# Kernel tuning notes

Hardware: AMD Instinct MI355X
Metric: run time of the kernel (lower is better)

Reference implementation:

```python
import jax, jax.numpy as jnp
import numpy as np

B, C, H, W = 2, 48, 64, 64
EPS = 1e-5
ROW = [0, 0, 0, H // 4, H // 4, H // 4, H // 2, H // 2, H // 2]
COL = [0, W // 4, W // 2] * 3


def setup_inputs() -> dict:
    key = jax.random.key(0)
    ks = iter(jax.random.split(key, 40))
    s = 1.0 / np.sqrt(C)  # keep unscaled-softmax logits sane
    def rn(shape, scale=1.0):
        return jax.random.normal(next(ks), shape, jnp.float32) * scale
    def ru(shape):
        return jax.random.uniform(next(ks), shape, jnp.float32, 0.5, 1.5)
    return dict(
        input_feature=rn((B, C, H, W)), feat_b=rn((B, C, H, W)),
        feat_c=rn((B, C, H, W)), feat_d=rn((B, C, H, W)),
        W_fa_all=rn((C, C), s), W_fb_all=rn((C, C), s),
        W_fc_all=rn((C, C), s), W_fd_all=rn((C, C), s),
        W_fa=rn((9, C, C), s), W_fb=rn((9, C, C), s),
        W_fc=rn((9, C, C), s), W_fd=rn((9, C, C), s),
        fuse_w=rn((C, 4 * C), s), fuse_b=rn((C,), 0.1),
        fuse_g=ru((C,)), fuse_bb=rn((C,), 0.1), fuse_m=rn((C,), 0.1), fuse_v=ru((C,)),
        fuseP_w=rn((9, C, 4 * C), s), fuseP_b=rn((9, C), 0.1),
        fuseP_g=ru((9, C)), fuseP_bb=rn((9, C), 0.1), fuseP_m=rn((9, C), 0.1), fuseP_v=ru((9, C)),
        gamma_all=rn(()), gamma_p=rn((9,)),
        out_w=rn((C, C, 3, 3), s / 3.0), out_b=rn((C,), 0.1),
        out_g=ru((C,)), out_bb=rn((C,), 0.1), out_m=rn((C,), 0.1), out_v=ru((C,)),
    )


def _attn(q, k, v):
    # q,k,v: [..., C, N] -> energy [..., N, N]; non-standard softmax(max - energy)
    e = jnp.einsum('...cn,...cm->...nm', q, k)
    e = jnp.max(e, axis=-1, keepdims=True) - e
    a = jax.nn.softmax(e, axis=-1)
    return jnp.einsum('...cn,...nm->...cm', v, a)  # torch.matmul(v, attention)


def reference(input_feature, feat_b, feat_c, feat_d,
              W_fa_all, W_fb_all, W_fc_all, W_fd_all,
              W_fa, W_fb, W_fc, W_fd,
              fuse_w, fuse_b, fuse_g, fuse_bb, fuse_m, fuse_v,
              fuseP_w, fuseP_b, fuseP_g, fuseP_bb, fuseP_m, fuseP_v,
              gamma_all, gamma_p,
              out_w, out_b, out_g, out_bb, out_m, out_v):
    h2, w2 = H // 2, W // 2
    N = H * W
    # ---- global branch: channel-wise Linear (bias=False) applied over spatial tokens
    fa = jnp.einsum('dc,bcn->bdn', W_fa_all, input_feature.reshape(B, C, N))
    fb = jnp.einsum('dc,bcn->bdn', W_fb_all, feat_b.reshape(B, C, N))
    fc = jnp.einsum('dc,bcn->bdn', W_fc_all, feat_c.reshape(B, C, N))
    fd = jnp.einsum('dc,bcn->bdn', W_fd_all, feat_d.reshape(B, C, N))
    cat = jnp.concatenate([_attn(fa, fa, fa), _attn(fa, fb, fb),
                           _attn(fa, fc, fc), _attn(fa, fd, fd)], axis=1)
    cat = cat.reshape(B, 4 * C, H, W)
    y = jnp.einsum('oc,bchw->bohw', fuse_w, cat) + fuse_b[None, :, None, None]
    y = (y - fuse_m[:, None, None]) * (fuse_g / jnp.sqrt(fuse_v + EPS))[:, None, None] + fuse_bb[:, None, None]
    atten_all = jax.nn.relu(y)  # Dropout2d is identity at eval
    # ---- 9 overlapping patch branches, vectorized over the patch axis p
    def crops(x):
        return jnp.stack([x[:, :, r:r + h2, c:c + w2] for r, c in zip(ROW, COL)], 0).reshape(9, B, C, h2 * w2)
    pa = jnp.einsum('pdc,pbcn->pbdn', W_fa, crops(input_feature))
    pb = jnp.einsum('pdc,pbcn->pbdn', W_fb, crops(feat_b))
    pc = jnp.einsum('pdc,pbcn->pbdn', W_fc, crops(feat_c))
    pd = jnp.einsum('pdc,pbcn->pbdn', W_fd, crops(feat_d))
    pcat = jnp.concatenate([_attn(pa, pa, pa), _attn(pa, pb, pb),
                            _attn(pa, pc, pc), _attn(pa, pd, pd)], axis=2)
    pcat = pcat.reshape(9, B, 4 * C, h2, w2)
    py = jnp.einsum('poc,pbchw->pbohw', fuseP_w, pcat) + fuseP_b[:, None, :, None, None]
    py = ((py - fuseP_m[:, None, :, None, None])
          * (fuseP_g / jnp.sqrt(fuseP_v + EPS))[:, None, :, None, None]
          + fuseP_bb[:, None, :, None, None])
    patch_out = 0.5 * gamma_p[:, None, None, None, None] * jax.nn.relu(py)
    # ---- combine (overlapping patch regions accumulate additively, as in torch +=)
    out = input_feature + gamma_all * atten_all
    for i, (r, c) in enumerate(zip(ROW, COL)):
        out = out.at[:, :, r:r + h2, c:c + w2].add(patch_out[i])
    # ---- to_out: 3x3 conv + BN(eval) + ReLU
    z = jax.lax.conv_general_dilated(out, out_w, (1, 1), 'SAME',
                                     dimension_numbers=('NCHW', 'OIHW', 'NCHW'))
    z = z + out_b[None, :, None, None]
    z = (z - out_m[:, None, None]) * (out_g / jnp.sqrt(out_v + EPS))[:, None, None] + out_bb[:, None, None]
    return jax.nn.relu(z)
```

## Files before the change

### kernel.cpp

```cpp
#include <hip/hip_runtime.h>
#include <math.h>

typedef _Float16 f16;
typedef f16 f16x8 __attribute__((ext_vector_type(8)));
typedef float f32x4 __attribute__((ext_vector_type(4)));

namespace {
constexpr int B_ = 2, C_ = 48, H_ = 64, W_ = 64;
constexpr int N_ = H_ * W_;
constexpr int NP_ = 1024;
constexpr int C4_ = 4 * C_;
constexpr float EPS_ = 1e-5f;
constexpr float L2E_ = 1.44269504f;
constexpr float REFL2_ = -25.0f * 1.44269504f;
}

#define MFMA32(a, b, c) __builtin_amdgcn_mfma_f32_16x16x32_f16((a), (b), (c), 0, 0, 0)

__device__ inline float fast_exp2(float x) {
#if __has_builtin(__builtin_amdgcn_exp2f)
  return __builtin_amdgcn_exp2f(x);
#else
  float r;
  asm("v_exp_f32 %0, %1" : "=v"(r) : "v"(x));
  return r;
#endif
}

__device__ __attribute__((always_inline)) void proj_body(
    const float* __restrict__ xb, const float* __restrict__ Ws,
    f16* __restrict__ pnb, size_t pn_stride, f16* __restrict__ ptb) {
  float acc[48];
#pragma unroll
  for (int d = 0; d < 48; ++d) acc[d] = 0.f;
  for (int c0 = 0; c0 < 48; c0 += 4) {
    float xv0 = xb[(size_t)(c0 + 0) * 4096];
    float xv1 = xb[(size_t)(c0 + 1) * 4096];
    float xv2 = xb[(size_t)(c0 + 2) * 4096];
    float xv3 = xb[(size_t)(c0 + 3) * 4096];
#pragma unroll
    for (int d = 0; d < 48; ++d) {
      const float4 wv = *(const float4*)&Ws[d * 48 + c0];
      acc[d] = fmaf(wv.x, xv0, fmaf(wv.y, xv1, fmaf(wv.z, xv2, fmaf(wv.w, xv3, acc[d]))));
    }
  }
#pragma unroll
  for (int d = 0; d < 48; ++d) pnb[(size_t)d * pn_stride] = (f16)acc[d];
#pragma unroll
  for (int s = 0; s < 6; ++s) {
    f16x8 v;
#pragma unroll
    for (int j = 0; j < 8; ++j) v[j] = (f16)acc[s * 8 + j];
    *(f16x8*)(ptb + s * 8) = v;
  }
  f16x8 zv = {0, 0, 0, 0, 0, 0, 0, 0};
  *(f16x8*)(ptb + 48) = zv;
  *(f16x8*)(ptb + 56) = zv;
}

__global__ __launch_bounds__(256) void k_proj_all(
    const float* __restrict__ x0, const float* __restrict__ x1,
    const float* __restrict__ x2, const float* __restrict__ x3,
    const float* __restrict__ w0, const float* __restrict__ w1,
    const float* __restrict__ w2, const float* __restrict__ w3,
    const float* __restrict__ wp0, const float* __restrict__ wp1,
    const float* __restrict__ wp2, const float* __restrict__ wp3,
    f16* __restrict__ pgn, f16* __restrict__ pgt,
    f16* __restrict__ ppn, f16* __restrict__ ppt) {
  __shared__ float Ws[48 * 48];
  int tid = threadIdx.x;
  int bid = blockIdx.x;
  if (bid < 128) {
    int bx = bid & 15, b = (bid >> 4) & 1, X = bid >> 5;
    const float* xp = X == 0 ? x0 : X == 1 ? x1 : X == 2 ? x2 : x3;
    const float* wp = X == 0 ? w0 : X == 1 ? w1 : X == 2 ? w2 : w3;
    for (int i = tid; i < 2304; i += 256) Ws[i] = wp[i];
    __syncthreads();
    int n = bx * 256 + tid;
    int z2 = X * 2 + b;
    proj_body(xp + (size_t)b * 48 * 4096 + n, Ws,
              pgn + ((size_t)z2 * 48) * 4096 + n, 4096,
              pgt + ((size_t)z2 * 4096 + n) * 64);
  } else {
    int pid = bid - 128;
    int bx = pid & 3;
    int rest = pid >> 2;
    int p = rest % 9;
    int zb = rest / 9;
    int X = zb >> 1, b = zb & 1;
    const float* xp = X == 0 ? x0 : X == 1 ? x1 : X == 2 ? x2 : x3;
    const float* wp = (X == 0 ? wp0 : X == 1 ? wp1 : X == 2 ? wp2 : wp3) + (size_t)p * 2304;
    for (int i = tid; i < 2304; i += 256) Ws[i] = wp[i];
    __syncthreads();
    int t = bx * 256 + tid;
    int r0 = (p / 3) * 16, c0w = (p % 3) * 16;
    int rr = r0 + (t >> 5), cc = c0w + (t & 31);
    int z9 = (X * 2 + b) * 9 + p;
    proj_body(xp + (size_t)b * 48 * 4096 + rr * 64 + cc, Ws,
              ppn + ((size_t)z9 * 48) * 1024 + t, 1024,
              ppt + ((size_t)z9 * 1024 + t) * 64);
  }
}

template <int NT, int NSPLIT, bool PATCH>
__device__ __attribute__((always_inline)) void stats_body(
    const f16* __restrict__ qT_all, const f16* __restrict__ kT_all,
    float* __restrict__ stp, int bx, int by, uint4* Ks) {
  constexpr int MTI = (NT / NSPLIT) / 64;
  int tid = threadIdx.x, wave = tid >> 6, lane = tid & 63, g = lane >> 4, lm = lane & 15;
  int ms = by % NSPLIT, z = by / NSPLIT;
  const f16* qT;
  if (PATCH) {
    int b = (z / 9) % 2, p = z % 9;
    qT = qT_all + ((size_t)(b * 9 + p)) * NT * 64;
  } else {
    int b = z & 1;
    qT = qT_all + (size_t)b * NT * 64;
  }
  const f16* kT = kT_all + (size_t)z * NT * 64;
  int n0 = bx * 128 + wave * 16;
  f16x8 aq0a = *(const f16x8*)(qT + (size_t)(n0 + lm) * 64 + g * 8);
  f16x8 aq1a = *(const f16x8*)(qT + (size_t)(n0 + lm) * 64 + 32 + g * 8);
  f16x8 aq0b = *(const f16x8*)(qT + (size_t)(n0 + 64 + lm) * 64 + g * 8);
  f16x8 aq1b = *(const f16x8*)(qT + (size_t)(n0 + 64 + lm) * 64 + 32 + g * 8);
  const int s0r = tid >> 3, s0c = (tid & 7) * 8;
  const int sw0 = tid ^ ((tid >> 3) & 7);
  const int sw1 = (tid + 256) ^ (((tid + 256) >> 3) & 7);
  const int swl = lm & 7;
  const int c0i = g ^ swl, c1i = (4 + g) ^ swl;
  int t_beg = ms * MTI;
  {
    const f16* src = kT + (size_t)t_beg * 64 * 64;
    Ks[sw0] = *(const uint4*)(src + (size_t)s0r * 64 + s0c);
    Ks[sw1] = *(const uint4*)(src + (size_t)(s0r + 32) * 64 + s0c);
  }
  __syncthreads();
  float zsa[4] = {0.f, 0.f, 0.f, 0.f};
  float zsb[4] = {0.f, 0.f, 0.f, 0.f};
  for (int mt = 0; mt < MTI; ++mt) {
    int cur = mt & 1;
    bool pf = (mt + 1 < MTI);
    uint4 k0v, k1v;
    if (pf) {
      const f16* src = kT + (size_t)(t_beg + mt + 1) * 64 * 64;
      k0v = *(const uint4*)(src + (size_t)s0r * 64 + s0c);
      k1v = *(const uint4*)(src + (size_t)(s0r + 32) * 64 + s0c);
    }
    uint4* kb = Ks + cur * 512;
#pragma unroll
    for (int mf = 0; mf < 4; ++mf) {
      f16x8 b0 = __builtin_bit_cast(f16x8, kb[(16 * mf + lm) * 8 + c0i]);
      f16x8 b1 = __builtin_bit_cast(f16x8, kb[(16 * mf + lm) * 8 + c1i]);
      f32x4 ea = {0.f, 0.f, 0.f, 0.f};
      ea = MFMA32(aq0a, b0, ea);
      ea = MFMA32(aq1a, b1, ea);
      f32x4 eb = {0.f, 0.f, 0.f, 0.f};
      eb = MFMA32(aq0b, b0, eb);
      eb = MFMA32(aq1b, b1, eb);
#pragma unroll
      for (int r = 0; r < 4; ++r) {
        zsa[r] += fast_exp2(fmaf(ea[r], -L2E_, REFL2_));
        zsb[r] += fast_exp2(fmaf(eb[r], -L2E_, REFL2_));
      }
    }
    if (pf) {
      uint4* kn = Ks + (cur ^ 1) * 512;
      kn[sw0] = k0v;
      kn[sw1] = k1v;
    }
    __syncthreads();
  }
#pragma unroll
  for (int mask = 1; mask < 16; mask <<= 1) {
#pragma unroll
    for (int r = 0; r < 4; ++r) {
      zsa[r] += __shfl_xor(zsa[r], mask, 64);
      zsb[r] += __shfl_xor(zsb[r], mask, 64);
    }
  }
  if (lm == 0) {
#pragma unroll
    for (int r = 0; r < 4; ++r) {
      stp[((size_t)z * NT + n0 + 4 * g + r) * NSPLIT + ms] = zsa[r];
      stp[((size_t)z * NT + n0 + 64 + 4 * g + r) * NSPLIT + ms] = zsb[r];
    }
  }
}

__global__ __launch_bounds__(256, 6) void k_stats_all(
    const f16* __restrict__ pg_t, float* __restrict__ stpg,
    const f16* __restrict__ pp_t, float* __restrict__ stpp) {
  __shared__ uint4 Ks[2 * 512];
  int bid = blockIdx.x;
  if (bid < 1024) {
    stats_body<N_, 4, false>(pg_t, pg_t, stpg, bid & 31, bid >> 5, Ks);
  } else {
    int pid = bid - 1024;
    stats_body<NP_, 1, true>(pp_t, pp_t, stpp, pid & 7, pid >> 3, Ks);
  }
}

__global__ __launch_bounds__(256) void k_merge_all(
    const float* __restrict__ stpg, float* __restrict__ stg,
    const float* __restrict__ stpp, float* __restrict__ stp2) {
  int i = blockIdx.x * 256 + threadIdx.x;
  if (i < 8 * N_) {
    const float* p = stpg + (size_t)i * 4;
    float Z = p[0] + p[1] + p[2] + p[3];
    stg[i] = REFL2_ - __log2f(Z);
  } else {
    int j = i - 8 * N_;
    if (j < 72 * NP_) stp2[j] = REFL2_ - __log2f(stpp[j]);
  }
}

template <int NT, int NSPLIT, bool PATCH>
__device__ __attribute__((always_inline)) void pv_body(
    const f16* __restrict__ qT_all, const f16* __restrict__ kT_all,
    const f16* __restrict__ vN_all, const float* __restrict__ st_all,
    float* __restrict__ out_all, int bx, int by,
    float* As2, uint4* Qs, uint4* Vs, uint2* wt2) {
  constexpr int CH = NT / NSPLIT;
  constexpr int NTI = CH / 64;
  int tid = threadIdx.x, wave = tid >> 6, lane = tid & 63, g = lane >> 4, lm = lane & 15;
  int ns = by % NSPLIT, z = by / NSPLIT;
  const f16 *qT, *kT, *vN;
  float* op;
  if (PATCH) {
    int X = z / 18, b = (z / 9) % 2, p = z % 9;
    qT = qT_all + ((size_t)(b * 9 + p)) * NT * 64;
    op = out_all + ((size_t)((p * 2 + b) * C4_ + X * 48)) * NT;
  } else {
    int X = z >> 1, b = z & 1;
    qT = qT_all + (size_t)b * NT * 64;
    op = out_all + ((size_t)(b * C4_ + X * 48)) * NT;
  }
  kT = kT_all + (size_t)z * NT * 64;
  vN = vN_all + (size_t)z * 48 * NT;
  const float* st = st_all + (size_t)z * NT + ns * CH;
  ((float4*)As2)[tid] = ((const float4*)st)[tid];
  int mwa = bx * 128 + wave * 16;
  int mwb = mwa + 64;
  f16x8 bk0a = *(const f16x8*)(kT + (size_t)(mwa + lm) * 64 + g * 8);
  f16x8 bk1a = *(const f16x8*)(kT + (size_t)(mwa + lm) * 64 + 32 + g * 8);
  f16x8 bk0b = *(const f16x8*)(kT + (size_t)(mwb + lm) * 64 + g * 8);
  f16x8 bk1b = *(const f16x8*)(kT + (size_t)(mwb + lm) * 64 + 32 + g * 8);
  const int s0r = tid >> 3, s0c = (tid & 7) * 8;
  const int sw0 = tid ^ ((tid >> 3) & 7);
  const int sw1 = (tid + 256) ^ (((tid + 256) >> 3) & 7);
  const int swl = lm & 7;
  const int c0i = g ^ swl, c1i = (4 + g) ^ swl;
  int t_beg = ns * NTI;
  {
    const f16* qsrc = qT + (size_t)t_beg * 64 * 64;
    Qs[sw0] = *(const uint4*)(qsrc + (size_t)s0r * 64 + s0c);
    Qs[sw1] = *(const uint4*)(qsrc + (size_t)(s0r + 32) * 64 + s0c);
    Vs[sw0] = *(const uint4*)(vN + (size_t)s0r * NT + t_beg * 64 + s0c);
    if (tid < 128)
      Vs[sw1] = *(const uint4*)(vN + (size_t)(s0r + 32) * NT + t_beg * 64 + s0c);
  }
  __syncthreads();
  f32x4 oa0 = {0.f, 0.f, 0.f, 0.f}, oa1 = {0.f, 0.f, 0.f, 0.f}, oa2 = {0.f, 0.f, 0.f, 0.f};
  f32x4 ob0 = {0.f, 0.f, 0.f, 0.f}, ob1 = {0.f, 0.f, 0.f, 0.f}, ob2 = {0.f, 0.f, 0.f, 0.f};
  int wbufa = wave * 512;
  int wbufb = wave * 512 + 256;
  int rba = wbufa + lm * 16;
  int rbb = wbufb + lm * 16;
  for (int nt = 0; nt < NTI; ++nt) {
    bool pf = (nt + 1 < NTI);
    uint4 q0v, q1v, v0v, v1v;
    if (pf) {
      int tn = t_beg + nt + 1;
      const f16* qsrc = qT + (size_t)tn * 64 * 64;
      q0v = *(const uint4*)(qsrc + (size_t)s0r * 64 + s0c);
      q1v = *(const uint4*)(qsrc + (size_t)(s0r + 32) * 64 + s0c);
      v0v = *(const uint4*)(vN + (size_t)s0r * NT + tn * 64 + s0c);
      if (tid < 128)
        v1v = *(const uint4*)(vN + (size_t)(s0r + 32) * NT + tn * 64 + s0c);
    }
    f32x4 ea[4], eb[4];
#pragma unroll
    for (int nf = 0; nf < 4; ++nf) {
      f16x8 a0 = __builtin_bit_cast(f16x8, Qs[(16 * nf + lm) * 8 + c0i]);
      f16x8 a1 = __builtin_bit_cast(f16x8, Qs[(16 * nf + lm) * 8 + c1i]);
      f32x4 ta = {0.f, 0.f, 0.f, 0.f};
      ta = MFMA32(a0, bk0a, ta);
      ta = MFMA32(a1, bk1a, ta);
      ea[nf] = ta;
      f32x4 tb = {0.f, 0.f, 0.f, 0.f};
      tb = MFMA32(a0, bk0b, tb);
      tb = MFMA32(a1, bk1b, tb);
      eb[nf] = tb;
    }
#pragma unroll
    for (int nf = 0; nf < 4; ++nf) {
      float4 a4 = *(const float4*)&As2[nt * 64 + nf * 16 + g * 4];
      float wa0 = fast_exp2(fmaf(ea[nf][0], -L2E_, a4.x));
      float wa1 = fast_exp2(fmaf(ea[nf][1], -L2E_, a4.y));
      float wa2 = fast_exp2(fmaf(ea[nf][2], -L2E_, a4.z));
      float wa3 = fast_exp2(fmaf(ea[nf][3], -L2E_, a4.w));
      float wb0 = fast_exp2(fmaf(eb[nf][0], -L2E_, a4.x));
      float wb1 = fast_exp2(fmaf(eb[nf][1], -L2E_, a4.y));
      float wb2 = fast_exp2(fmaf(eb[nf][2], -L2E_, a4.z));
      float wb3 = fast_exp2(fmaf(eb[nf][3], -L2E_, a4.w));
      unsigned la = __builtin_bit_cast(unsigned, __builtin_amdgcn_cvt_pkrtz(wa0, wa1));
      unsigned ha = __builtin_bit_cast(unsigned, __builtin_amdgcn_cvt_pkrtz(wa2, wa3));
      unsigned lb = __builtin_bit_cast(unsigned, __builtin_amdgcn_cvt_pkrtz(wb0, wb1));
      unsigned hb = __builtin_bit_cast(unsigned, __builtin_amdgcn_cvt_pkrtz(wb2, wb3));
      int s = 2 * nf + (g >> 1);
      int so = ((s ^ swl) * 2) + (g & 1);
      wt2[wbufa + lm * 16 + so] = make_uint2(la, ha);
      wt2[wbufb + lm * 16 + so] = make_uint2(lb, hb);
    }
    __builtin_amdgcn_sched_barrier(0);
    f16x8 bw0a = __builtin_bit_cast(f16x8, *(const uint4*)&wt2[rba + c0i * 2]);
    f16x8 bw1a = __builtin_bit_cast(f16x8, *(const uint4*)&wt2[rba + c1i * 2]);
    f16x8 bw0b = __builtin_bit_cast(f16x8, *(const uint4*)&wt2[rbb + c0i * 2]);
    f16x8 bw1b = __builtin_bit_cast(f16x8, *(const uint4*)&wt2[rbb + c1i * 2]);
#pragma unroll
    for (int cf = 0; cf < 3; ++cf) {
      f16x8 av0 = __builtin_bit_cast(f16x8, Vs[(16 * cf + lm) * 8 + c0i]);
      f16x8 av1 = __builtin_bit_cast(f16x8, Vs[(16 * cf + lm) * 8 + c1i]);
      if (cf == 0) {
        oa0 = MFMA32(av0, bw0a, oa0); oa0 = MFMA32(av1, bw1a, oa0);
        ob0 = MFMA32(av0, bw0b, ob0); ob0 = MFMA32(av1, bw1b, ob0);
      }
      if (cf == 1) {
        oa1 = MFMA32(av0, bw0a, oa1); oa1 = MFMA32(av1, bw1a, oa1);
        ob1 = MFMA32(av0, bw0b, ob1); ob1 = MFMA32(av1, bw1b, ob1);
      }
      if (cf == 2) {
        oa2 = MFMA32(av0, bw0a, oa2); oa2 = MFMA32(av1, bw1a, oa2);
        ob2 = MFMA32(av0, bw0b, ob2); ob2 = MFMA32(av1, bw1b, ob2);
      }
    }
    __syncthreads();
    if (pf) {
      Qs[sw0] = q0v;
      Qs[sw1] = q1v;
      Vs[sw0] = v0v;
      if (tid < 128) Vs[sw1] = v1v;
    }
    __syncthreads();
  }
  if (NSPLIT == 1) {
#pragma unroll
    for (int r = 0; r < 4; ++r) {
      op[(size_t)(0 + 4 * g + r) * NT + mwa + lm] = oa0[r];
      op[(size_t)(16 + 4 * g + r) * NT + mwa + lm] = oa1[r];
      op[(size_t)(32 + 4 * g + r) * NT + mwa + lm] = oa2[r];
      op[(size_t)(0 + 4 * g + r) * NT + mwb + lm] = ob0[r];
      op[(size_t)(16 + 4 * g + r) * NT + mwb + lm] = ob1[r];
      op[(size_t)(32 + 4 * g + r) * NT + mwb + lm] = ob2[r];
    }
  } else {
#pragma unroll
    for (int r = 0; r < 4; ++r) {
      atomicAdd(&op[(size_t)(0 + 4 * g + r) * NT + mwa + lm], oa0[r]);
      atomicAdd(&op[(size_t)(16 + 4 * g + r) * NT + mwa + lm], oa1[r]);
      atomicAdd(&op[(size_t)(32 + 4 * g + r) * NT + mwa + lm], oa2[r]);
      atomicAdd(&op[(size_t)(0 + 4 * g + r) * NT + mwb + lm], ob0[r]);
      atomicAdd(&op[(size_t)(16 + 4 * g + r) * NT + mwb + lm], ob1[r]);
      atomicAdd(&op[(size_t)(32 + 4 * g + r) * NT + mwb + lm], ob2[r]);
    }
  }
}

__global__ __launch_bounds__(256, 4) void k_pv_all(
    const f16* __restrict__ pg_t, const f16* __restrict__ pg_n,
    const float* __restrict__ statsg, float* __restrict__ cat,
    const f16* __restrict__ pp_t, const f16* __restrict__ pp_n,
    const float* __restrict__ statsp, float* __restrict__ pcat) {
  __shared__ float As2[1024];
  __shared__ uint4 Qs[512];
  __shared__ uint4 Vs[384];
  __shared__ uint2 wt2[2048];
  int bid = blockIdx.x;
  if (bid < 1024) {
    pv_body<N_, 4, false>(pg_t, pg_t, pg_n, statsg, cat, bid & 31, bid >> 5,
                          As2, Qs, Vs, wt2);
  } else {
    int pid = bid - 1024;
    pv_body<NP_, 1, true>(pp_t, pp_t, pp_n, statsp, pcat, pid & 7, pid >> 3,
                          As2, Qs, Vs, wt2);
  }
}

__global__ __launch_bounds__(256) void k_fuse_all(
    const float* __restrict__ cat, const float* __restrict__ fw,
    const float* __restrict__ fb, const float* __restrict__ fg,
    const float* __restrict__ fbb, const float* __restrict__ fm,
    const float* __restrict__ fv, const float* __restrict__ gamma_all,
    const float* __restrict__ input, float* __restrict__ comb,
    const float* __restrict__ pcat, const float* __restrict__ pfw,
    const float* __restrict__ pfb, const float* __restrict__ pfg,
    const float* __restrict__ pfbb, const float* __restrict__ pfm,
    const float* __restrict__ pfv, const float* __restrict__ gamma_p,
    float* __restrict__ py) {
  int bid = blockIdx.x;
  if (bid < 384) {
    int idx = bid * 256 + threadIdx.x;
    int n4 = idx & 1023;
    int rest = idx >> 10;
    int o = rest % C_;
    int b = rest / C_;
    const float* cr = cat + (size_t)b * C4_ * N_ + n4 * 4;
    const float* wr = fw + (size_t)o * C4_;
    float4 acc = {0.f, 0.f, 0.f, 0.f};
#pragma unroll 8
    for (int c = 0; c < C4_; ++c) {
      float4 xv = *(const float4*)(cr + (size_t)c * N_);
      float w = wr[c];
      acc.x = fmaf(w, xv.x, acc.x); acc.y = fmaf(w, xv.y, acc.y);
      acc.z = fmaf(w, xv.z, acc.z); acc.w = fmaf(w, xv.w, acc.w);
    }
    float scale = fg[o] * rsqrtf(fv[o] + EPS_);
    float sh = fb[o] - fm[o], bb = fbb[o], ga = gamma_all[0];
    float4 inv = *(const float4*)(input + ((size_t)(b * C_ + o) * N_) + n4 * 4);
    float4 out;
    out.x = inv.x + ga * fmaxf((acc.x + sh) * scale + bb, 0.f);
    out.y = inv.y + ga * fmaxf((acc.y + sh) * scale + bb, 0.f);
    out.z = inv.z + ga * fmaxf((acc.z + sh) * scale + bb, 0.f);
    out.w = inv.w + ga * fmaxf((acc.w + sh) * scale + bb, 0.f);
    *(float4*)(comb + ((size_t)(b * C_ + o) * N_) + n4 * 4) = out;
  } else {
    int idx = (bid - 384) * 256 + threadIdx.x;
    int t4 = idx & 255;
    int rest = idx >> 8;
    int o = rest % C_; rest /= C_;
    int b = rest % B_;
    int p = rest / B_;
    const float* cr = pcat + ((size_t)(p * B_ + b) * C4_) * NP_ + t4 * 4;
    const float* wr = pfw + (size_t)(p * C_ + o) * C4_;
    float4 acc = {0.f, 0.f, 0.f, 0.f};
#pragma unroll 8
    for (int c = 0; c < C4_; ++c) {
      float4 xv = *(const float4*)(cr + (size_t)c * NP_);
      float w = wr[c];
      acc.x = fmaf(w, xv.x, acc.x); acc.y = fmaf(w, xv.y, acc.y);
      acc.z = fmaf(w, xv.z, acc.z); acc.w = fmaf(w, xv.w, acc.w);
    }
    int po = p * C_ + o;
    float scale = pfg[po] * rsqrtf(pfv[po] + EPS_);
    float sh = pfb[po] - pfm[po], bb = pfbb[po], gp = 0.5f * gamma_p[p];
    float4 out;
    out.x = gp * fmaxf((acc.x + sh) * scale + bb, 0.f);
    out.y = gp * fmaxf((acc.y + sh) * scale + bb, 0.f);
    out.z = gp * fmaxf((acc.z + sh) * scale + bb, 0.f);
    out.w = gp * fmaxf((acc.w + sh) * scale + bb, 0.f);
    *(float4*)(py + ((size_t)(p * B_ + b) * C_ + o) * NP_ + t4 * 4) = out;
  }
}

__global__ __launch_bounds__(256) void k_combine(
    const float* __restrict__ py, const float* __restrict__ comb,
    f16* __restrict__ combh) {
  int idx = blockIdx.x * 256 + threadIdx.x;
  int w = idx & (W_ - 1);
  int h = (idx >> 6) & (H_ - 1);
  int rest = idx >> 12;
  int ch = rest % C_;
  int b = rest / C_;
  float val = comb[idx];
#pragma unroll
  for (int p = 0; p < 9; ++p) {
    int r0 = (p / 3) * 16, c0 = (p % 3) * 16;
    if (h >= r0 && h < r0 + 32 && w >= c0 && w < c0 + 32)
      val += py[((size_t)(p * B_ + b) * C_ + ch) * NP_ + (h - r0) * 32 + (w - c0)];
  }
  combh[idx] = (f16)val;
}

__global__ __launch_bounds__(256) void k_conv2(
    const f16* __restrict__ combh, const float* __restrict__ cw,
    const float* __restrict__ cb, const float* __restrict__ cg,
    const float* __restrict__ cbb, const float* __restrict__ cm,
    const float* __restrict__ cv, float* __restrict__ out) {
  __shared__ uint4 inh[2304];
  int tid = threadIdx.x;
  int h0 = blockIdx.x * 4, ocg = blockIdx.y, b = blockIdx.z;
  for (int i = tid; i < 2304; i += 256) {
    int c = i / 48;
    int rem = i - c * 48;
    int r = rem >> 3, u = rem & 7;
    int hh = h0 - 1 + r;
    uint4 val = make_uint4(0, 0, 0, 0);
    if (hh >= 0 && hh < H_)
      val = *(const uint4*)(combh + (((size_t)(b * C_ + c) * H_ + hh) * W_ + u * 8));
    inh[i] = val;
  }
  __syncthreads();
  int w = tid & 63, dh = tid >> 6;
  float acc[6] = {0.f, 0.f, 0.f, 0.f, 0.f, 0.f};
  const f16* lds = (const f16*)inh;
  int wm = w > 0 ? w - 1 : 0;
  int wp = w < 63 ? w + 1 : 63;
  for (int c = 0; c < 48; ++c) {
    float v[9];
#pragma unroll
    for (int r = 0; r < 3; ++r) {
      const f16* row = lds + (size_t)(c * 6 + dh + r) * 64;
      float lf = (float)row[wm];
      float md = (float)row[w];
      float rt = (float)row[wp];
      v[r * 3 + 0] = (w > 0) ? lf : 0.f;
      v[r * 3 + 1] = md;
      v[r * 3 + 2] = (w < 63) ? rt : 0.f;
    }
#pragma unroll
    for (int j = 0; j < 6; ++j) {
      const float* wr = cw + (size_t)((ocg * 6 + j) * 48 + c) * 9;
#pragma unroll
      for (int k = 0; k < 9; ++k) acc[j] = fmaf(v[k], wr[k], acc[j]);
    }
  }
#pragma unroll
  for (int j = 0; j < 6; ++j) {
    int o = ocg * 6 + j;
    float scale = cg[o] * rsqrtf(cv[o] + EPS_);
    float y = (acc[j] + cb[o] - cm[o]) * scale + cbb[o];
    out[(size_t)(b * C_ + o) * N_ + (h0 + dh) * 64 + w] = fmaxf(y, 0.f);
  }
}

extern "C" void kernel_launch(void* const* d_in, const int* in_sizes, int n_in,
                              void* d_out, int out_size, void* d_ws, size_t ws_size,
                              hipStream_t stream) {
  (void)in_sizes; (void)n_in; (void)out_size; (void)ws_size;
  const float* x[4];
  const float* Wall[4];
  const float* Wp[4];
  for (int i = 0; i < 4; ++i) {
    x[i] = (const float*)d_in[i];
    Wall[i] = (const float*)d_in[4 + i];
    Wp[i] = (const float*)d_in[8 + i];
  }
  const float* fuse_w = (const float*)d_in[12];
  const float* fuse_b = (const float*)d_in[13];
  const float* fuse_g = (const float*)d_in[14];
  const float* fuse_bb = (const float*)d_in[15];
  const float* fuse_m = (const float*)d_in[16];
  const float* fuse_v = (const float*)d_in[17];
  const float* fuseP_w = (const float*)d_in[18];
  const float* fuseP_b = (const float*)d_in[19];
  const float* fuseP_g = (const float*)d_in[20];
  const float* fuseP_bb = (const float*)d_in[21];
  const float* fuseP_m = (const float*)d_in[22];
  const float* fuseP_v = (const float*)d_in[23];
  const float* gamma_all = (const float*)d_in[24];
  const float* gamma_p = (const float*)d_in[25];
  const float* out_w = (const float*)d_in[26];
  const float* out_b = (const float*)d_in[27];
  const float* out_g = (const float*)d_in[28];
  const float* out_bb = (const float*)d_in[29];
  const float* out_m = (const float*)d_in[30];
  const float* out_v = (const float*)d_in[31];

  char* base = (char*)d_ws;
  size_t off = 0;
  auto carve = [&](size_t bytes) {
    char* p = base + off;
    off += (bytes + 255) & ~(size_t)255;
    return p;
  };
  f16* projg_n = (f16*)carve((size_t)8 * 48 * N_ * 2);
  f16* projg_t = (f16*)carve((size_t)8 * N_ * 64 * 2);
  f16* projp_n = (f16*)carve((size_t)72 * 48 * NP_ * 2);
  f16* projp_t = (f16*)carve((size_t)72 * NP_ * 64 * 2);
  float* stpg = (float*)carve((size_t)8 * N_ * 4 * 4);
  float* stpp = (float*)carve((size_t)72 * NP_ * 4);
  float* statsg = (float*)carve((size_t)8 * N_ * 4);
  float* statsp = (float*)carve((size_t)72 * NP_ * 4);
  float* cat = (float*)carve((size_t)B_ * C4_ * N_ * 4);
  float* pcat = (float*)carve((size_t)9 * B_ * C4_ * NP_ * 4);
  float* comb = (float*)carve((size_t)B_ * C_ * N_ * 4);
  float* py = (float*)carve((size_t)9 * B_ * C_ * NP_ * 4);
  f16* combh = (f16*)carve((size_t)B_ * C_ * N_ * 2);

  dim3 blk(256);

  (void)hipMemsetAsync(cat, 0, (size_t)B_ * C4_ * N_ * sizeof(float), stream);
  k_proj_all<<<dim3(416), blk, 0, stream>>>(
      x[0], x[1], x[2], x[3], Wall[0], Wall[1], Wall[2], Wall[3],
      Wp[0], Wp[1], Wp[2], Wp[3], projg_n, projg_t, projp_n, projp_t);

  k_stats_all<<<dim3(1600), blk, 0, stream>>>(projg_t, stpg, projp_t, stpp);
  k_merge_all<<<dim3((8 * N_ + 72 * NP_ + 255) / 256), blk, 0, stream>>>(
      stpg, statsg, stpp, statsp);

  k_pv_all<<<dim3(1600), blk, 0, stream>>>(
      projg_t, projg_n, statsg, cat, projp_t, projp_n, statsp, pcat);

  k_fuse_all<<<dim3(1248), blk, 0, stream>>>(
      cat, fuse_w, fuse_b, fuse_g, fuse_bb, fuse_m, fuse_v, gamma_all, x[0], comb,
      pcat, fuseP_w, fuseP_b, fuseP_g, fuseP_bb, fuseP_m, fuseP_v, gamma_p, py);
  k_combine<<<(B_ * C_ * N_) / 256, blk, 0, stream>>>(py, comb, combh);
  k_conv2<<<dim3(16, 8, 2), blk, 0, stream>>>(
      combh, out_w, out_b, out_g, out_bb, out_m, out_v, (float*)d_out);
}
```

Baseline: 240.2 us.

## Fuse patch scatter-add into fuse kernel via atomics and add MFMA priority hints

```diff
diff --git a/kernel.cpp b/kernel.cpp
--- a/kernel.cpp
+++ b/kernel.cpp
@@ -147,6 +147,7 @@
       k1v = *(const uint4*)(src + (size_t)(s0r + 32) * 64 + s0c);
     }
     uint4* kb = Ks + cur * 512;
+    __builtin_amdgcn_s_setprio(1);
 #pragma unroll
     for (int mf = 0; mf < 4; ++mf) {
       f16x8 b0 = __builtin_bit_cast(f16x8, kb[(16 * mf + lm) * 8 + c0i]);
@@ -163,6 +164,7 @@
         zsb[r] += fast_exp2(fmaf(eb[r], -L2E_, REFL2_));
       }
     }
+    __builtin_amdgcn_s_setprio(0);
     if (pf) {
       uint4* kn = Ks + (cur ^ 1) * 512;
       kn[sw0] = k0v;
@@ -279,6 +281,7 @@
         v1v = *(const uint4*)(vN + (size_t)(s0r + 32) * NT + tn * 64 + s0c);
     }
     f32x4 ea[4], eb[4];
+    __builtin_amdgcn_s_setprio(1);
 #pragma unroll
     for (int nf = 0; nf < 4; ++nf) {
       f16x8 a0 = __builtin_bit_cast(f16x8, Qs[(16 * nf + lm) * 8 + c0i]);
@@ -292,6 +295,7 @@
       tb = MFMA32(a1, bk1b, tb);
       eb[nf] = tb;
     }
+    __builtin_amdgcn_s_setprio(0);
 #pragma unroll
     for (int nf = 0; nf < 4; ++nf) {
       float4 a4 = *(const float4*)&As2[nt * 64 + nf * 16 + g * 4];
@@ -317,6 +321,7 @@
     f16x8 bw1a = __builtin_bit_cast(f16x8, *(const uint4*)&wt2[rba + c1i * 2]);
     f16x8 bw0b = __builtin_bit_cast(f16x8, *(const uint4*)&wt2[rbb + c0i * 2]);
     f16x8 bw1b = __builtin_bit_cast(f16x8, *(const uint4*)&wt2[rbb + c1i * 2]);
+    __builtin_amdgcn_s_setprio(1);
 #pragma unroll
     for (int cf = 0; cf < 3; ++cf) {
       f16x8 av0 = __builtin_bit_cast(f16x8, Vs[(16 * cf + lm) * 8 + c0i]);
@@ -334,6 +339,7 @@
         ob2 = MFMA32(av0, bw0b, ob2); ob2 = MFMA32(av1, bw1b, ob2);
       }
     }
+    __builtin_amdgcn_s_setprio(0);
     __syncthreads();
     if (pf) {
       Qs[sw0] = q0v;
@@ -395,8 +401,7 @@
     const float* __restrict__ pcat, const float* __restrict__ pfw,
     const float* __restrict__ pfb, const float* __restrict__ pfg,
     const float* __restrict__ pfbb, const float* __restrict__ pfm,
-    const float* __restrict__ pfv, const float* __restrict__ gamma_p,
-    float* __restrict__ py) {
+    const float* __restrict__ pfv, const float* __restrict__ gamma_p) {
   int bid = blockIdx.x;
   if (bid < 384) {
     int idx = bid * 256 + threadIdx.x;
@@ -417,12 +422,11 @@
     float scale = fg[o] * rsqrtf(fv[o] + EPS_);
     float sh = fb[o] - fm[o], bb = fbb[o], ga = gamma_all[0];
     float4 inv = *(const float4*)(input + ((size_t)(b * C_ + o) * N_) + n4 * 4);
-    float4 out;
-    out.x = inv.x + ga * fmaxf((acc.x + sh) * scale + bb, 0.f);
-    out.y = inv.y + ga * fmaxf((acc.y + sh) * scale + bb, 0.f);
-    out.z = inv.z + ga * fmaxf((acc.z + sh) * scale + bb, 0.f);
-    out.w = inv.w + ga * fmaxf((acc.w + sh) * scale + bb, 0.f);
-    *(float4*)(comb + ((size_t)(b * C_ + o) * N_) + n4 * 4) = out;
+    float* base = comb + ((size_t)(b * C_ + o) * N_) + n4 * 4;
+    atomicAdd(base + 0, inv.x + ga * fmaxf((acc.x + sh) * scale + bb, 0.f));
+    atomicAdd(base + 1, inv.y + ga * fmaxf((acc.y + sh) * scale + bb, 0.f));
+    atomicAdd(base + 2, inv.z + ga * fmaxf((acc.z + sh) * scale + bb, 0.f));
+    atomicAdd(base + 3, inv.w + ga * fmaxf((acc.w + sh) * scale + bb, 0.f));
   } else {
     int idx = (bid - 384) * 256 + threadIdx.x;
     int t4 = idx & 255;
@@ -443,66 +447,49 @@
     int po = p * C_ + o;
     float scale = pfg[po] * rsqrtf(pfv[po] + EPS_);
     float sh = pfb[po] - pfm[po], bb = pfbb[po], gp = 0.5f * gamma_p[p];
-    float4 out;
-    out.x = gp * fmaxf((acc.x + sh) * scale + bb, 0.f);
-    out.y = gp * fmaxf((acc.y + sh) * scale + bb, 0.f);
-    out.z = gp * fmaxf((acc.z + sh) * scale + bb, 0.f);
-    out.w = gp * fmaxf((acc.w + sh) * scale + bb, 0.f);
-    *(float4*)(py + ((size_t)(p * B_ + b) * C_ + o) * NP_ + t4 * 4) = out;
-  }
-}
-
-__global__ __launch_bounds__(256) void k_combine(
-    const float* __restrict__ py, const float* __restrict__ comb,
-    f16* __restrict__ combh) {
-  int idx = blockIdx.x * 256 + threadIdx.x;
-  int w = idx & (W_ - 1);
-  int h = (idx >> 6) & (H_ - 1);
-  int rest = idx >> 12;
-  int ch = rest % C_;
-  int b = rest / C_;
-  float val = comb[idx];
-#pragma unroll
-  for (int p = 0; p < 9; ++p) {
-    int r0 = (p / 3) * 16, c0 = (p % 3) * 16;
-    if (h >= r0 && h < r0 + 32 && w >= c0 && w < c0 + 32)
-      val += py[((size_t)(p * B_ + b) * C_ + ch) * NP_ + (h - r0) * 32 + (w - c0)];
-  }
-  combh[idx] = (f16)val;
+    int t = t4 * 4;
+    int r0 = (p / 3) * 16, c0w = (p % 3) * 16;
+    int h = r0 + (t >> 5), w = c0w + (t & 31);
+    float* base = comb + ((size_t)(b * C_ + o) * N_) + h * 64 + w;
+    atomicAdd(base + 0, gp * fmaxf((acc.x + sh) * scale + bb, 0.f));
+    atomicAdd(base + 1, gp * fmaxf((acc.y + sh) * scale + bb, 0.f));
+    atomicAdd(base + 2, gp * fmaxf((acc.z + sh) * scale + bb, 0.f));
+    atomicAdd(base + 3, gp * fmaxf((acc.w + sh) * scale + bb, 0.f));
+  }
 }
 
 __global__ __launch_bounds__(256) void k_conv2(
-    const f16* __restrict__ combh, const float* __restrict__ cw,
+    const float* __restrict__ comb, const float* __restrict__ cw,
     const float* __restrict__ cb, const float* __restrict__ cg,
     const float* __restrict__ cbb, const float* __restrict__ cm,
     const float* __restrict__ cv, float* __restrict__ out) {
-  __shared__ uint4 inh[2304];
+  __shared__ float4 inh[4608];
   int tid = threadIdx.x;
   int h0 = blockIdx.x * 4, ocg = blockIdx.y, b = blockIdx.z;
-  for (int i = tid; i < 2304; i += 256) {
-    int c = i / 48;
-    int rem = i - c * 48;
-    int r = rem >> 3, u = rem & 7;
+  for (int i = tid; i < 4608; i += 256) {
+    int c = i / 96;
+    int rem = i - c * 96;
+    int r = rem >> 4, u = rem & 15;
     int hh = h0 - 1 + r;
-    uint4 val = make_uint4(0, 0, 0, 0);
+    float4 val = make_float4(0.f, 0.f, 0.f, 0.f);
     if (hh >= 0 && hh < H_)
-      val = *(const uint4*)(combh + (((size_t)(b * C_ + c) * H_ + hh) * W_ + u * 8));
+      val = *(const float4*)(comb + (((size_t)(b * C_ + c) * H_ + hh) * W_ + u * 4));
     inh[i] = val;
   }
   __syncthreads();
   int w = tid & 63, dh = tid >> 6;
   float acc[6] = {0.f, 0.f, 0.f, 0.f, 0.f, 0.f};
-  const f16* lds = (const f16*)inh;
+  const float* lds = (const float*)inh;
   int wm = w > 0 ? w - 1 : 0;
   int wp = w < 63 ? w + 1 : 63;
   for (int c = 0; c < 48; ++c) {
     float v[9];
 #pragma unroll
     for (int r = 0; r < 3; ++r) {
-      const f16* row = lds + (size_t)(c * 6 + dh + r) * 64;
-      float lf = (float)row[wm];
-      float md = (float)row[w];
-      float rt = (float)row[wp];
+      const float* row = lds + (size_t)(c * 6 + dh + r) * 64;
+      float lf = row[wm];
+      float md = row[w];
+      float rt = row[wp];
       v[r * 3 + 0] = (w > 0) ? lf : 0.f;
       v[r * 3 + 1] = md;
       v[r * 3 + 2] = (w < 63) ? rt : 0.f;
@@ -574,12 +561,11 @@
   float* cat = (float*)carve((size_t)B_ * C4_ * N_ * 4);
   float* pcat = (float*)carve((size_t)9 * B_ * C4_ * NP_ * 4);
   float* comb = (float*)carve((size_t)B_ * C_ * N_ * 4);
-  float* py = (float*)carve((size_t)9 * B_ * C_ * NP_ * 4);
-  f16* combh = (f16*)carve((size_t)B_ * C_ * N_ * 2);
 
   dim3 blk(256);
 
   (void)hipMemsetAsync(cat, 0, (size_t)B_ * C4_ * N_ * sizeof(float), stream);
+  (void)hipMemsetAsync(comb, 0, (size_t)B_ * C_ * N_ * sizeof(float), stream);
   k_proj_all<<<dim3(416), blk, 0, stream>>>(
       x[0], x[1], x[2], x[3], Wall[0], Wall[1], Wall[2], Wall[3],
       Wp[0], Wp[1], Wp[2], Wp[3], projg_n, projg_t, projp_n, projp_t);
@@ -593,8 +579,7 @@
 
   k_fuse_all<<<dim3(1248), blk, 0, stream>>>(
       cat, fuse_w, fuse_b, fuse_g, fuse_bb, fuse_m, fuse_v, gamma_all, x[0], comb,
-      pcat, fuseP_w, fuseP_b, fuseP_g, fuseP_bb, fuseP_m, fuseP_v, gamma_p, py);
-  k_combine<<<(B_ * C_ * N_) / 256, blk, 0, stream>>>(py, comb, combh);
+      pcat, fuseP_w, fuseP_b, fuseP_g, fuseP_bb, fuseP_m, fuseP_v, gamma_p);
   k_conv2<<<dim3(16, 8, 2), blk, 0, stream>>>(
-      combh, out_w, out_b, out_g, out_bb, out_m, out_v, (float*)d_out);
-}
+      comb, out_w, out_b, out_g, out_bb, out_m, out_v, (float*)d_out);
+}
```

After: 240.7 us. Within noise of the previous version (+0.2%).
